# Optimization experiments

Hardware: AMD Instinct MI355X
Metric: run time of the kernel (lower is better)

The kernel has to match this reference:

```python
import jax, jax.numpy as jnp
import numpy as np

N_LAYERS = 2
DIN = 128
DOUT = 128


def _uniform(key, shape, std):
    return jax.random.uniform(key, shape, jnp.float32, -std, std)


def setup_inputs() -> dict:
    key = jax.random.key(0)
    ks = jax.random.split(key, 12)
    B, T, N, F = 2, 8, 10000, DIN
    E = 320000
    x = jax.random.normal(ks[0], (B, T, N, F), jnp.float32)
    edge_index = jax.random.randint(ks[1], (2, E), 0, N, jnp.int64)
    edge_weight = jax.random.uniform(ks[2], (E,), jnp.float32)
    std_w = 1.0 / np.sqrt(DOUT)
    std_p = 1.0 / np.sqrt(DIN)
    std_g = 1.0 / np.sqrt(DIN)  # torch GRUCell init: U(-1/sqrt(H), 1/sqrt(H))
    W0 = _uniform(ks[3], (N_LAYERS, DIN, DOUT), std_w)
    p = _uniform(ks[4], (N_LAYERS, DIN, 1), std_p)
    w_ih = _uniform(ks[5], (N_LAYERS, 3 * DIN, DIN), std_g)
    w_hh = _uniform(ks[6], (N_LAYERS, 3 * DIN, DIN), std_g)
    b_ih = _uniform(ks[7], (N_LAYERS, 3 * DIN), std_g)
    b_hh = _uniform(ks[8], (N_LAYERS, 3 * DIN), std_g)
    bias = jnp.zeros((N_LAYERS, DOUT), jnp.float32)
    return {"x": x, "edge_index": edge_index, "edge_weight": edge_weight,
            "W0": W0, "p": p, "w_ih": w_ih, "w_hh": w_hh,
            "b_ih": b_ih, "b_hh": b_hh, "bias": bias}


def _gru_cell(xg, hg, wih, whh, bih, bhh):
    # torch.nn.GRUCell: gate order r, z, n
    gi = xg @ wih.T + bih
    gh = hg @ whh.T + bhh
    ir, iz, inn = jnp.split(gi, 3, axis=-1)
    hr, hz, hn = jnp.split(gh, 3, axis=-1)
    r = jax.nn.sigmoid(ir + hr)
    z = jax.nn.sigmoid(iz + hz)
    n = jnp.tanh(inn + r * hn)
    return (1.0 - z) * n + z * hg


def _topk_pool(xb, pc, k):
    # xb: [b, N, din], pc: [din, 1] -> [b, k, din]
    scores = (xb @ pc)[..., 0] / jnp.linalg.norm(pc)  # [b, N]
    vals, idx = jax.lax.top_k(scores, k)               # [b, k], sorted desc
    g = jnp.take_along_axis(xb, idx[..., None], axis=1)  # [b, k, din]
    return g * jnp.tanh(vals)[..., None]


def reference(x, edge_index, edge_weight, W0, p, w_ih, w_hh, b_ih, b_hh, bias):
    B, T, N, F = x.shape
    dout = W0.shape[-1]
    # --- GCN symmetric normalization with self-loops (done once, static graph) ---
    src, tgt = edge_index[0], edge_index[1]
    loops = jnp.arange(N, dtype=src.dtype)
    row = jnp.concatenate([src, loops])
    col = jnp.concatenate([tgt, loops])
    w = jnp.concatenate([edge_weight, jnp.ones((N,), x.dtype)])
    deg = jnp.zeros((N,), x.dtype).at[col].add(w)
    dinv = jnp.where(deg > 0, deg ** -0.5, 0.0)
    wn = dinv[row] * w * dinv[col]  # [E+N]

    def step(Ws, xt):
        out = xt  # [b, N, din]
        new_Ws = []
        for c in range(N_LAYERS):
            W = Ws[c]  # [b, din, dout]
            din = W.shape[1]
            pooled = _topk_pool(out, p[c], dout)                 # [b, dout, din]
            hg = W.transpose(0, 2, 1).reshape(B * dout, din)     # (b dout) din
            xg = pooled.reshape(B * dout, din)
            hg = _gru_cell(xg, hg, w_ih[c], w_hh[c], b_ih[c], b_hh[c])
            W = hg.reshape(B, dout, din).transpose(0, 2, 1)      # [b, din, dout]
            o = jnp.einsum('bnd,bde->bne', out, W)               # [b, N, dout]
            # gather-scale-scatter propagation (aggr='add')
            m = o[:, row, :] * wn[None, :, None]                 # [b, E+N, dout]
            o = jnp.zeros((B, N, dout), x.dtype).at[:, col, :].add(m)
            o = o + bias[c]
            out = jax.nn.relu(o)
            new_Ws.append(W)
        return tuple(new_Ws), out

    Ws0 = tuple(jnp.broadcast_to(W0[c], (B,) + W0[c].shape) for c in range(N_LAYERS))
    _, outs = jax.lax.scan(step, Ws0, jnp.moveaxis(x, 1, 0))
    return outs[-1]  # output at final step, [b, N, hidden]
```

## Files before the change

### kernel.cpp

```cpp
#include <hip/hip_runtime.h>
#include <hip/hip_bf16.h>
#include <math.h>


#define BB 2
#define TT 8
#define FF 128
#define GG 384
#define BINS 8192
#define CAP 512

typedef float v4f __attribute__((ext_vector_type(4)));

__device__ __forceinline__ float bf2f(unsigned short u) {
  return __uint_as_float((unsigned)u << 16);
}
__device__ __forceinline__ unsigned short f2bf(float f) {
  unsigned x = __float_as_uint(f);
  unsigned r = ((x >> 16) & 1u) + 0x7fffu;
  return (unsigned short)((x + r) >> 16);
}

__global__ void prep_kernel(const int* __restrict__ ei32, int E, int* __restrict__ flag,
                            const float* __restrict__ p, float* __restrict__ pinv) {
  if (blockIdx.x == 0) {
    int step = E / 256;
    int e = threadIdx.x * step;
    if (ei32[2 * e + 1] != 0) *flag = 1;
  } else {
    int c = blockIdx.x - 1, tid = threadIdx.x;
    float s = 0.f;
    if (tid < 128) { float v = p[c * FF + tid]; s = v * v; }
    for (int o = 32; o; o >>= 1) s += __shfl_xor(s, o, 64);
    __shared__ float red[4];
    if ((tid & 63) == 0) red[tid >> 6] = s;
    __syncthreads();
    if (tid == 0) pinv[c] = 1.0f / sqrtf(red[0] + red[1] + red[2] + red[3]);
  }
}

__device__ __forceinline__ void edge_fetch(const void* ei, int is32, int E,
                                           int e, const float* ew,
                                           int& row, int& col, float& w) {
  if (e < E) {
    if (is32) {
      const int* p = (const int*)ei;
      row = p[e]; col = p[E + e];
    } else {
      const long long* p = (const long long*)ei;
      row = (int)p[e]; col = (int)p[(long long)E + e];
    }
    w = ew[e];
  } else {
    row = col = e - E; w = 1.0f;
  }
}

__global__ void hist_kernel(const void* ei, const int* flag, int E, int N,
                            const float* __restrict__ ew,
                            float* __restrict__ deg, int* __restrict__ counts) {
  int e = blockIdx.x * 256 + threadIdx.x;
  if (e >= E + N) return;
  int row, col; float w;
  edge_fetch(ei, *flag, E, e, ew, row, col, w);
  atomicAdd(&deg[col], w);
  atomicAdd(&counts[col], 1);
}

__global__ __launch_bounds__(1024) void scan_kernel(
    const int* __restrict__ counts, const float* __restrict__ deg,
    int* __restrict__ offsets, float* __restrict__ dinv, int N, int EN) {
  __shared__ int wtot[16];
  int tid = threadIdx.x, lane = tid & 63, wid = tid >> 6;
  int base = tid * 10;
  int lc[10]; int s10 = 0;
#pragma unroll
  for (int q = 0; q < 10; ++q) {
    int idx = base + q;
    int cv = (idx < N) ? counts[idx] : 0;
    lc[q] = cv; s10 += cv;
    if (idx < N) {
      float d = deg[idx];
      dinv[idx] = (d > 0.f) ? 1.0f / sqrtf(d) : 0.f;
    }
  }
  int s = s10;
#pragma unroll
  for (int off = 1; off <= 32; off <<= 1) {
    int v = __shfl_up(s, off, 64);
    if (lane >= off) s += v;
  }
  if (lane == 63) wtot[wid] = s;
  __syncthreads();
  int pre = 0;
  for (int w2 = 0; w2 < wid; ++w2) pre += wtot[w2];
  int run = pre + s - s10;
#pragma unroll
  for (int q = 0; q < 10; ++q) {
    int idx = base + q;
    if (idx < N) { offsets[idx] = run; run += lc[q]; }
  }
  if (tid == 0) offsets[N] = EN;
}

__global__ void scatter_kernel(const void* ei, const int* flag, int E, int N,
                               const float* __restrict__ ew,
                               const float* __restrict__ dinv,
                               const int* __restrict__ offs,
                               int* __restrict__ cursors,
                               int2* __restrict__ ep) {
  int e = blockIdx.x * 256 + threadIdx.x;
  if (e >= E + N) return;
  int row, col; float w;
  edge_fetch(ei, *flag, E, e, ew, row, col, w);
  int pos = atomicAdd(&cursors[col], 1);
  ep[offs[col] + pos] = make_int2(row, __float_as_int(dinv[row] * w * dinv[col]));
}

template <int SRC_BF16>
__global__ __launch_bounds__(256) void prop_kernel(
    const void* __restrict__ srcv, size_t s_tstride, size_t s_bstride,
    float* __restrict__ dst, size_t d_tstride, size_t d_bstride,
    const int2* __restrict__ ep, const int* __restrict__ offs,
    const float* __restrict__ p, const float* __restrict__ pinv,
    unsigned long long* __restrict__ keys, int* __restrict__ hist,
    int N, int NG, int t8) {
  constexpr int PER = SRC_BF16 ? 8 : 4;
  constexpr int RSU = SRC_BF16 ? 16 : 32;
  int lid = blockIdx.x;
  int t, s;
  if (t8) { t = lid & 7; s = lid >> 3; } else { t = 0; s = lid; }
  int fq = s / NG, vg = s - fq * NG;
  int lane = threadIdx.x & 63;
  int e = lane >> 3, sub = lane & 7;
  int v = vg * 4 + (threadIdx.x >> 6);
  if (v >= N) return;
  int e0 = offs[v], e1 = offs[v + 1];
  size_t o0 = (size_t)t * s_tstride, o1 = o0 + s_bstride;
  const uint4* g0;
  const uint4* g1;
  if constexpr (SRC_BF16) {
    g0 = (const uint4*)((const unsigned short*)srcv + o0);
    g1 = (const uint4*)((const unsigned short*)srcv + o1);
  } else {
    g0 = (const uint4*)((const float*)srcv + o0);
    g1 = (const uint4*)((const float*)srcv + o1);
  }
  int fqs = fq * 8;
  float acc0[PER], acc1[PER];
#pragma unroll
  for (int q = 0; q < PER; ++q) { acc0[q] = 0.f; acc1[q] = 0.f; }
  for (int base = e0; base < e1; base += 64) {
    int cnt = e1 - base; if (cnt > 64) cnt = 64;
    int2 m = make_int2(0, 0);
    if (lane < cnt) m = ep[base + lane];
    for (int i = 0; i < cnt; i += 8) {
      int srcl = i + e;
      int row = __shfl(m.x, srcl, 64);
      float wv = __int_as_float(__shfl(m.y, srcl, 64));
      if (srcl >= cnt) wv = 0.f;
      size_t r = (size_t)row * RSU + fqs + sub;
      uint4 ra = g0[r], rb = g1[r];
      if constexpr (SRC_BF16) {
        acc0[0] += wv * bf2f(ra.x & 0xffff); acc0[1] += wv * bf2f(ra.x >> 16);
        acc0[2] += wv * bf2f(ra.y & 0xffff); acc0[3] += wv * bf2f(ra.y >> 16);
        acc0[4] += wv * bf2f(ra.z & 0xffff); acc0[5] += wv * bf2f(ra.z >> 16);
        acc0[6] += wv * bf2f(ra.w & 0xffff); acc0[7] += wv * bf2f(ra.w >> 16);
        acc1[0] += wv * bf2f(rb.x & 0xffff); acc1[1] += wv * bf2f(rb.x >> 16);
        acc1[2] += wv * bf2f(rb.y & 0xffff); acc1[3] += wv * bf2f(rb.y >> 16);
        acc1[4] += wv * bf2f(rb.z & 0xffff); acc1[5] += wv * bf2f(rb.z >> 16);
        acc1[6] += wv * bf2f(rb.w & 0xffff); acc1[7] += wv * bf2f(rb.w >> 16);
      } else {
        acc0[0] += wv * __uint_as_float(ra.x);
        acc0[1] += wv * __uint_as_float(ra.y);
        acc0[2] += wv * __uint_as_float(ra.z);
        acc0[3] += wv * __uint_as_float(ra.w);
        acc1[0] += wv * __uint_as_float(rb.x);
        acc1[1] += wv * __uint_as_float(rb.y);
        acc1[2] += wv * __uint_as_float(rb.z);
        acc1[3] += wv * __uint_as_float(rb.w);
      }
    }
  }
#pragma unroll
  for (int mk = 8; mk <= 32; mk <<= 1) {
#pragma unroll
    for (int q = 0; q < PER; ++q) {
      acc0[q] += __shfl_xor(acc0[q], mk, 64);
      acc1[q] += __shfl_xor(acc1[q], mk, 64);
    }
  }
  if (e < 2) {
    float* ob = dst + (size_t)t * d_tstride + (e ? d_bstride : 0);
    float* av = e ? acc1 : acc0;
    size_t fo = (size_t)v * FF + fq * (PER * 8) + sub * PER;
    v4f st0 = {av[0], av[1], av[2], av[3]};
    __builtin_nontemporal_store(st0, (v4f*)(ob + fo));
    if constexpr (SRC_BF16) {
      v4f st1 = {av[4], av[5], av[6], av[7]};
      __builtin_nontemporal_store(st1, (v4f*)(ob + fo + 4));
    }
  }
  if constexpr (!SRC_BF16) {
    if (p && fq == 0) {
      int half = lane >> 5, i32 = lane & 31;
      const v4f* xrow = (const v4f*)(half ? g1 : g0);
      v4f xv = __builtin_nontemporal_load(xrow + (size_t)v * 32 + i32);
      float4 pp = ((const float4*)p)[i32];
      float sc = xv.x * pp.x + xv.y * pp.y + xv.z * pp.z + xv.w * pp.w;
#pragma unroll
      for (int o = 1; o <= 16; o <<= 1) sc += __shfl_xor(sc, o, 64);
      if (i32 == 0) {
        float ss = sc * (*pinv);
        unsigned u = __float_as_uint(ss);
        u = (u & 0x80000000u) ? ~u : (u | 0x80000000u);
        int tb = t * 2 + half;
        keys[(size_t)tb * N + v] = ((unsigned long long)u << 32) | (unsigned)(~v);
        atomicAdd(&hist[tb * BINS + (u >> 19)], 1);
      }
    }
  }
}

__device__ __forceinline__ unsigned long long shfl_xor_u64(unsigned long long x,
                                                           int m) {
  unsigned lo = (unsigned)x, hi = (unsigned)(x >> 32);
  lo = __shfl_xor(lo, m, 64);
  hi = __shfl_xor(hi, m, 64);
  return ((unsigned long long)hi << 32) | lo;
}

__global__ __launch_bounds__(1024) void selectsort_kernel(
    const unsigned long long* __restrict__ keys, const int* __restrict__ hist,
    int N, int* __restrict__ idx_sel, float* __restrict__ gate_sel) {
  int tb = blockIdx.y * 2 + blockIdx.x, tid = threadIdx.x;
  int lane = tid & 63, wid = tid >> 6;
  const int* h = hist + tb * BINS;
  __shared__ int wtot[16];
  __shared__ unsigned long long cand[CAP];
  __shared__ int sT, ncnt;
  int base = tid * 8;
  int lc[8]; int local = 0;
#pragma unroll
  for (int q = 0; q < 8; ++q) { lc[q] = h[base + q]; local += lc[q]; }
  if (tid == 0) ncnt = 0;
  int s = local;
#pragma unroll
  for (int off = 1; off <= 32; off <<= 1) {
    int v = __shfl_down(s, off, 64);
    if (lane + off < 64) s += v;
  }
  if (lane == 0) wtot[wid] = s;
  __syncthreads();
  int above_w = 0;
  for (int w2 = wid + 1; w2 < 16; ++w2) above_w += wtot[w2];
  int incl = above_w + s;
  int above = incl - local;
  if (above < 128 && incl >= 128) {
    int cnt = above;
#pragma unroll
    for (int q = 7; q >= 0; --q) {
      int c = lc[q];
      if (cnt + c >= 128) { sT = base + q; break; }
      cnt += c;
    }
  }
  __syncthreads();
  int T = sT;
  for (int i = tid; i < N; i += 1024) {
    unsigned long long kk = keys[(size_t)tb * N + i];
    if ((int)(kk >> 51) >= T) {
      int pos = atomicAdd(&ncnt, 1);
      if (pos < CAP) cand[pos] = kk;
    }
  }
  __syncthreads();
  if (tid < 64) {
    int nc = ncnt < CAP ? ncnt : CAP;
    unsigned long long v[8];
#pragma unroll
    for (int r = 0; r < 8; ++r) {
      int e = r * 64 + lane;
      v[r] = (e < nc) ? cand[e] : 0ULL;
    }
    for (int k = 2; k <= 512; k <<= 1)
      for (int j = k >> 1; j > 0; j >>= 1) {
        if (j >= 64) {
          int rj = j >> 6;
#pragma unroll
          for (int r = 0; r < 8; ++r)
            if (!(r & rj)) {
              int r2 = r | rj;
              bool up = (((r * 64) & k) != 0);
              unsigned long long a = v[r], c = v[r2];
              bool sw = up ? (a > c) : (a < c);
              if (sw) { v[r] = c; v[r2] = a; }
            }
        } else {
#pragma unroll
          for (int r = 0; r < 8; ++r) {
            unsigned long long o = shfl_xor_u64(v[r], j);
            int e = r * 64 + lane;
            bool up = (e & k) != 0;
            bool lower = (lane & j) == 0;
            unsigned long long mn = v[r] < o ? v[r] : o;
            unsigned long long mx = v[r] < o ? o : v[r];
            v[r] = (lower == up) ? mn : mx;
          }
        }
      }
#pragma unroll
    for (int r = 0; r < 2; ++r) {
      int e = r * 64 + lane;
      unsigned long long kk = v[r];
      unsigned n = ~((unsigned)kk);
      unsigned u = (unsigned)(kk >> 32);
      float sc = (u & 0x80000000u) ? __uint_as_float(u & 0x7FFFFFFFu)
                                   : __uint_as_float(~u);
      idx_sel[tb * 128 + e] = (int)n;
      gate_sel[tb * 128 + e] = tanhf(sc);
    }
  }
}

template <int SRC_BF16>
__global__ __launch_bounds__(256) void wchain_kernel(
    const void* __restrict__ srcv, size_t src_tstride, size_t src_bstride,
    const int* __restrict__ idx_sel, const float* __restrict__ gate_sel,
    const float* __restrict__ Winit,
    const float* __restrict__ wih, const float* __restrict__ whh,
    const float* __restrict__ bih, const float* __restrict__ bhh,
    float* __restrict__ snap) {
  int b = blockIdx.x, j0 = blockIdx.y * 2;
  int tid = threadIdx.x, side = tid >> 7, kl = tid & 127;
  __shared__ float pooled[2][FF];
  __shared__ float hbuf[2][FF];
  __shared__ float ghbuf[3][2][FF];
  for (int e = tid; e < 2 * FF; e += 256) {
    int j = e >> 7, m = e & 127;
    hbuf[j][m] = Winit[m * FF + j0 + j];
  }
  float b0 = side ? bhh[kl] : bih[kl];
  float b1 = side ? bhh[FF + kl] : bih[FF + kl];
  float b2 = side ? bhh[2 * FF + kl] : bih[2 * FF + kl];
  const float* wmat = side ? whh : wih;
  const float4* w0p = (const float4*)(wmat + (size_t)(0 * FF + kl) * FF);
  const float4* w1p = (const float4*)(wmat + (size_t)(1 * FF + kl) * FF);
  const float4* w2p = (const float4*)(wmat + (size_t)(2 * FF + kl) * FF);
  for (int t = 0; t < TT; ++t) {
    int tb = t * 2 + b;
    __syncthreads();
    for (int e = tid; e < 2 * FF; e += 256) {
      int j = e >> 7, m = e & 127;
      int n = idx_sel[tb * 128 + j0 + j];
      float g = gate_sel[tb * 128 + j0 + j];
      size_t off = (size_t)t * src_tstride + (size_t)b * src_bstride +
                   (size_t)n * FF + m;
      float xv;
      if constexpr (SRC_BF16) xv = bf2f(((const unsigned short*)srcv)[off]);
      else                    xv = ((const float*)srcv)[off];
      pooled[j][m] = xv * g;
    }
    __syncthreads();
    const float4* vsrc = (const float4*)(side ? &hbuf[0][0] : &pooled[0][0]);
    float acc0[2] = {}, acc1[2] = {}, acc2[2] = {};
    for (int mq = 0; mq < 32; ++mq) {
      float4 w0 = w0p[mq], w1 = w1p[mq], w2 = w2p[mq];
#pragma unroll
      for (int j = 0; j < 2; ++j) {
        float4 v = vsrc[j * 32 + mq];
        acc0[j] += v.x * w0.x + v.y * w0.y + v.z * w0.z + v.w * w0.w;
        acc1[j] += v.x * w1.x + v.y * w1.y + v.z * w1.z + v.w * w1.w;
        acc2[j] += v.x * w2.x + v.y * w2.y + v.z * w2.z + v.w * w2.w;
      }
    }
    if (side) {
#pragma unroll
      for (int j = 0; j < 2; ++j) {
        ghbuf[0][j][kl] = acc0[j] + b0;
        ghbuf[1][j][kl] = acc1[j] + b1;
        ghbuf[2][j][kl] = acc2[j] + b2;
      }
    }
    __syncthreads();
    if (!side) {
#pragma unroll
      for (int j = 0; j < 2; ++j) {
        float rr = 1.0f / (1.0f + expf(-(acc0[j] + b0 + ghbuf[0][j][kl])));
        float zz = 1.0f / (1.0f + expf(-(acc1[j] + b1 + ghbuf[1][j][kl])));
        float nn = tanhf(acc2[j] + b2 + rr * ghbuf[2][j][kl]);
        float h = hbuf[j][kl];
        float hn = (1.0f - zz) * nn + zz * h;
        hbuf[j][kl] = hn;
        snap[((size_t)tb * FF + kl) * FF + j0 + j] = hn;
      }
    }
  }
}

__global__ __launch_bounds__(256) void gemm_kernel(
    const float* __restrict__ A, size_t a_tstride, size_t a_bstride,
    const float* __restrict__ Wsnap, const float* __restrict__ bias,
    float* __restrict__ outf, unsigned short* __restrict__ outb,
    size_t o_tstride, size_t o_bstride,
    const float* __restrict__ p1, const float* __restrict__ pinv1,
    unsigned long long* __restrict__ keys, int* __restrict__ hist, int N) {
  int nb = blockIdx.x, b = blockIdx.y, t = blockIdx.z;
  int tb = t * 2 + b;
  __shared__ float As[128][33];
  __shared__ float Bs[32][128];
  __shared__ float spart[128][17];
  __shared__ float p1s[128];
  int tid = threadIdx.x;
  int tc = tid & 15, tr = tid >> 4;
  if (p1 && tid < 128) p1s[tid] = p1[tid];
  float acc[8][8] = {};
  const float* Ab = A + (size_t)t * a_tstride + (size_t)b * a_bstride;
  const float* Wb = Wsnap + (size_t)tb * FF * FF;
  for (int kc = 0; kc < 4; ++kc) {
    int k0 = kc * 32;
    __syncthreads();
    for (int e = tid; e < 128 * 32; e += 256) {
      int r = e >> 5, kk = e & 31;
      int n = nb * 128 + r;
      As[r][kk] = (n < N) ? Ab[(size_t)n * FF + k0 + kk] : 0.f;
    }
    for (int e = tid; e < 32 * 128; e += 256) {
      int r = e >> 7, dd = e & 127;
      Bs[r][dd] = Wb[(k0 + r) * FF + dd];
    }
    __syncthreads();
#pragma unroll 4
    for (int kk = 0; kk < 32; ++kk) {
      float av[8];
#pragma unroll
      for (int i = 0; i < 8; ++i) av[i] = As[tr * 8 + i][kk];
      const float4* brow = (const float4*)Bs[kk];
      float4 b0 = brow[tc * 2], b1 = brow[tc * 2 + 1];
      float bv[8] = {b0.x, b0.y, b0.z, b0.w, b1.x, b1.y, b1.z, b1.w};
#pragma unroll
      for (int i = 0; i < 8; ++i)
#pragma unroll
        for (int j = 0; j < 8; ++j) acc[i][j] += av[i] * bv[j];
    }
  }
  float bb[8];
#pragma unroll
  for (int j = 0; j < 8; ++j) bb[j] = bias[tc * 8 + j];
  size_t obase = (size_t)t * o_tstride + (size_t)b * o_bstride;
#pragma unroll
  for (int i = 0; i < 8; ++i) {
    int n = nb * 128 + tr * 8 + i;
    float v[8]; float part = 0.f;
#pragma unroll
    for (int j = 0; j < 8; ++j) {
      v[j] = fmaxf(acc[i][j] + bb[j], 0.f);
      if (p1) part += v[j] * p1s[tc * 8 + j];
    }
    if (n < N) {
      if (outb) {
        unsigned short* dst = outb + obase + (size_t)n * FF + tc * 8;
        uint4 pk;
        pk.x = (unsigned)f2bf(v[0]) | ((unsigned)f2bf(v[1]) << 16);
        pk.y = (unsigned)f2bf(v[2]) | ((unsigned)f2bf(v[3]) << 16);
        pk.z = (unsigned)f2bf(v[4]) | ((unsigned)f2bf(v[5]) << 16);
        pk.w = (unsigned)f2bf(v[6]) | ((unsigned)f2bf(v[7]) << 16);
        *(uint4*)dst = pk;
      } else {
        float4* dst = (float4*)(outf + obase + (size_t)n * FF + tc * 8);
        dst[0] = make_float4(v[0], v[1], v[2], v[3]);
        dst[1] = make_float4(v[4], v[5], v[6], v[7]);
      }
    }
    if (p1) spart[tr * 8 + i][tc] = part;
  }
  if (p1) {
    __syncthreads();
    if (tid < 128) {
      int n = nb * 128 + tid;
      if (n < N) {
        float s = 0.f;
#pragma unroll
        for (int q = 0; q < 16; ++q) s += spart[tid][q];
        s *= *pinv1;
        unsigned u = __float_as_uint(s);
        u = (u & 0x80000000u) ? ~u : (u | 0x80000000u);
        keys[(size_t)tb * N + n] = ((unsigned long long)u << 32) | (unsigned)(~n);
        atomicAdd(&hist[tb * BINS + (u >> 19)], 1);
      }
    }
  }
}

extern "C" void kernel_launch(void* const* d_in, const int* in_sizes, int n_in,
                              void* d_out, int out_size, void* d_ws, size_t ws_size,
                              hipStream_t stream) {
  const float* x   = (const float*)d_in[0];
  const void*  ei  = d_in[1];
  const float* ew  = (const float*)d_in[2];
  const float* W0  = (const float*)d_in[3];
  const float* p   = (const float*)d_in[4];
  const float* wih = (const float*)d_in[5];
  const float* whh = (const float*)d_in[6];
  const float* bih = (const float*)d_in[7];
  const float* bhh = (const float*)d_in[8];
  const float* bias= (const float*)d_in[9];

  const int E  = in_sizes[2];
  const int N  = in_sizes[0] / (BB * TT * FF);
  const int EN = E + N;
  const size_t NF = (size_t)N * FF;
  const int NG = (N + 3) / 4;

  char* w = (char*)d_ws;
  auto alloc = [&](size_t bytes) -> char* {
    char* r = w; w += (bytes + 255) & ~(size_t)255; return r;
  };
  char* zbeg = w;
  float* deg      = (float*)alloc((size_t)N * 4);
  int*   counts   = (int*)  alloc((size_t)N * 4);
  int*   cursors  = (int*)  alloc((size_t)N * 4);
  int*   flag     = (int*)  alloc(4);
  int*   hist     = (int*)  alloc((size_t)2 * TT * BB * BINS * 4);
  char* zend = w;
  int*   offsets  = (int*)  alloc((size_t)(N + 1) * 4);
  float* dinv     = (float*)alloc((size_t)N * 4);
  float* pinv     = (float*)alloc(2 * 4);
  int2*  ep       = (int2*) alloc((size_t)EN * 8);
  unsigned long long* keys0 = (unsigned long long*)alloc((size_t)TT * BB * N * 8);
  unsigned long long* keys1 = (unsigned long long*)alloc((size_t)TT * BB * N * 8);
  int*   idx0     = (int*)  alloc((size_t)TT * BB * 128 * 4);
  float* gate0    = (float*)alloc((size_t)TT * BB * 128 * 4);
  int*   idx1     = (int*)  alloc((size_t)TT * BB * 128 * 4);
  float* gate1    = (float*)alloc((size_t)TT * BB * 128 * 4);
  float* W0snap   = (float*)alloc((size_t)TT * BB * FF * FF * 4);
  float* W1snap   = (float*)alloc((size_t)TT * BB * FF * FF * 4);
  float* xp       = (float*)alloc((size_t)TT * BB * NF * 4);
  unsigned short* act0 = (unsigned short*)alloc((size_t)TT * BB * NF * 2);
  float* xq       = (float*)alloc((size_t)BB * NF * 4);
  int* hist0 = hist;
  int* hist1 = hist + (size_t)TT * BB * BINS;

  hipMemsetAsync(zbeg, 0, (size_t)(zend - zbeg), stream);

  prep_kernel<<<3, 256, 0, stream>>>((const int*)ei, E, flag, p, pinv);
  hist_kernel<<<(EN + 255) / 256, 256, 0, stream>>>(ei, flag, E, N, ew, deg, counts);
  scan_kernel<<<1, 1024, 0, stream>>>(counts, deg, offsets, dinv, N, EN);
  scatter_kernel<<<(EN + 255) / 256, 256, 0, stream>>>(ei, flag, E, N, ew, dinv,
                                                       offsets, cursors, ep);

  prop_kernel<0><<<NG * 4 * TT, 256, 0, stream>>>(
      x, NF, (size_t)TT * NF, xp, (size_t)BB * NF, NF,
      ep, offsets, p, pinv, keys0, hist0, N, NG, 1);

  selectsort_kernel<<<dim3(BB, TT), 1024, 0, stream>>>(
      keys0, hist0, N, idx0, gate0);

  wchain_kernel<0><<<dim3(BB, 64), 256, 0, stream>>>(
      x, NF, (size_t)TT * NF, idx0, gate0, W0,
      wih, whh, bih, bhh, W0snap);

  gemm_kernel<<<dim3((N + 127) / 128, BB, TT), 256, 0, stream>>>(
      xp, (size_t)BB * NF, NF, W0snap, bias,
      nullptr, act0, (size_t)BB * NF, NF,
      p + FF, pinv + 1, keys1, hist1, N);

  selectsort_kernel<<<dim3(BB, TT), 1024, 0, stream>>>(
      keys1, hist1, N, idx1, gate1);

  wchain_kernel<1><<<dim3(BB, 64), 256, 0, stream>>>(
      act0, (size_t)BB * NF, NF, idx1, gate1, W0 + FF * FF,
      wih + (size_t)GG * FF, whh + (size_t)GG * FF,
      bih + GG, bhh + GG, W1snap);

  prop_kernel<1><<<NG * 2, 256, 0, stream>>>(
      act0 + (size_t)(TT - 1) * BB * NF, 0, NF, xq, 0, NF,
      ep, offsets, nullptr, nullptr, nullptr, nullptr, N, NG, 0);

  gemm_kernel<<<dim3((N + 127) / 128, BB, 1), 256, 0, stream>>>(
      xq, 0, NF, W1snap + (size_t)(TT - 1) * BB * FF * FF, bias + FF,
      (float*)d_out, nullptr, 0, NF,
      nullptr, nullptr, nullptr, nullptr, N);
}
```

Measured before the change: 823.3 us.

## Split GRU weight chain into batched input-gate GEMM and lightweight recurrent kernel

The input-side GRU projection (pooled @ w_ih^T + b_ih) does not depend on the recurrent state, so it is hoisted out of the sequential time loop into a separate tiled GEMM kernel covering all timesteps and batches at once. The remaining recurrent kernel only computes the hidden-side projection and the gate math, using one column per block and 384 threads across all three gates. This gives more parallelism and less work on the serial chain. The cost is an extra launch and a global buffer round-trip for the precomputed input gates.

```diff
diff --git a/kernel.cpp b/kernel.cpp
--- a/kernel.cpp
+++ b/kernel.cpp
@@ -324,77 +324,105 @@
 }
 
 template <int SRC_BF16>
-__global__ __launch_bounds__(256) void wchain_kernel(
+__global__ __launch_bounds__(256) void gipre_kernel(
     const void* __restrict__ srcv, size_t src_tstride, size_t src_bstride,
     const int* __restrict__ idx_sel, const float* __restrict__ gate_sel,
+    const float* __restrict__ wih, const float* __restrict__ bih,
+    float* __restrict__ gi) {
+  int g = blockIdx.x, b = blockIdx.y, t = blockIdx.z;
+  int tb = t * 2 + b, gbase = g * 128;
+  __shared__ float As[128][33];
+  __shared__ float Bs[128][33];
+  __shared__ int s_idx[128];
+  __shared__ float s_gate[128];
+  int tid = threadIdx.x;
+  int tc = tid & 15, tr = tid >> 4;
+  if (tid < 128) {
+    s_idx[tid] = idx_sel[tb * 128 + tid];
+    s_gate[tid] = gate_sel[tb * 128 + tid];
+  }
+  float acc[8][8] = {};
+  const char* srcb = (const char*)srcv;
+  size_t sbase = (size_t)t * src_tstride + (size_t)b * src_bstride;
+  for (int kc = 0; kc < 4; ++kc) {
+    int k0 = kc * 32;
+    __syncthreads();
+    for (int e = tid; e < 128 * 32; e += 256) {
+      int j = e >> 5, kk = e & 31;
+      size_t off = sbase + (size_t)s_idx[j] * FF + k0 + kk;
+      float xv;
+      if constexpr (SRC_BF16) xv = bf2f(((const unsigned short*)srcb)[off]);
+      else                    xv = ((const float*)srcb)[off];
+      As[j][kk] = xv * s_gate[j];
+    }
+    for (int e = tid; e < 128 * 32; e += 256) {
+      int r = e >> 5, kk = e & 31;
+      Bs[r][kk] = wih[(size_t)(gbase + r) * FF + k0 + kk];
+    }
+    __syncthreads();
+#pragma unroll 4
+    for (int kk = 0; kk < 32; ++kk) {
+      float av[8], bv[8];
+#pragma unroll
+      for (int i = 0; i < 8; ++i) av[i] = As[tr * 8 + i][kk];
+#pragma unroll
+      for (int j = 0; j < 8; ++j) bv[j] = Bs[tc * 8 + j][kk];
+#pragma unroll
+      for (int i = 0; i < 8; ++i)
+#pragma unroll
+        for (int j = 0; j < 8; ++j) acc[i][j] += av[i] * bv[j];
+    }
+  }
+  float bb[8];
+#pragma unroll
+  for (int j = 0; j < 8; ++j) bb[j] = bih[gbase + tc * 8 + j];
+#pragma unroll
+  for (int i = 0; i < 8; ++i) {
+    float* dst = gi + (size_t)(tb * 128 + tr * 8 + i) * GG + gbase + tc * 8;
+    float4* d4 = (float4*)dst;
+    d4[0] = make_float4(acc[i][0] + bb[0], acc[i][1] + bb[1],
+                        acc[i][2] + bb[2], acc[i][3] + bb[3]);
+    d4[1] = make_float4(acc[i][4] + bb[4], acc[i][5] + bb[5],
+                        acc[i][6] + bb[6], acc[i][7] + bb[7]);
+  }
+}
+
+__global__ __launch_bounds__(384) void wlite_kernel(
+    const float* __restrict__ gi,
     const float* __restrict__ Winit,
-    const float* __restrict__ wih, const float* __restrict__ whh,
-    const float* __restrict__ bih, const float* __restrict__ bhh,
+    const float* __restrict__ whh, const float* __restrict__ bhh,
     float* __restrict__ snap) {
-  int b = blockIdx.x, j0 = blockIdx.y * 2;
-  int tid = threadIdx.x, side = tid >> 7, kl = tid & 127;
-  __shared__ float pooled[2][FF];
-  __shared__ float hbuf[2][FF];
-  __shared__ float ghbuf[3][2][FF];
-  for (int e = tid; e < 2 * FF; e += 256) {
-    int j = e >> 7, m = e & 127;
-    hbuf[j][m] = Winit[m * FF + j0 + j];
-  }
-  float b0 = side ? bhh[kl] : bih[kl];
-  float b1 = side ? bhh[FF + kl] : bih[FF + kl];
-  float b2 = side ? bhh[2 * FF + kl] : bih[2 * FF + kl];
-  const float* wmat = side ? whh : wih;
-  const float4* w0p = (const float4*)(wmat + (size_t)(0 * FF + kl) * FF);
-  const float4* w1p = (const float4*)(wmat + (size_t)(1 * FF + kl) * FF);
-  const float4* w2p = (const float4*)(wmat + (size_t)(2 * FF + kl) * FF);
+  int b = blockIdx.x, j = blockIdx.y;
+  int tid = threadIdx.x, g = tid >> 7, k = tid & 127;
+  __shared__ float hbuf[FF];
+  __shared__ float gh3[3][FF];
+  if (tid < 128) hbuf[tid] = Winit[tid * FF + j];
+  float bh = bhh[g * 128 + k];
+  const float4* wrow = (const float4*)(whh + (size_t)(g * 128 + k) * FF);
+  __syncthreads();
   for (int t = 0; t < TT; ++t) {
     int tb = t * 2 + b;
-    __syncthreads();
-    for (int e = tid; e < 2 * FF; e += 256) {
-      int j = e >> 7, m = e & 127;
-      int n = idx_sel[tb * 128 + j0 + j];
-      float g = gate_sel[tb * 128 + j0 + j];
-      size_t off = (size_t)t * src_tstride + (size_t)b * src_bstride +
-                   (size_t)n * FF + m;
-      float xv;
-      if constexpr (SRC_BF16) xv = bf2f(((const unsigned short*)srcv)[off]);
-      else                    xv = ((const float*)srcv)[off];
-      pooled[j][m] = xv * g;
-    }
-    __syncthreads();
-    const float4* vsrc = (const float4*)(side ? &hbuf[0][0] : &pooled[0][0]);
-    float acc0[2] = {}, acc1[2] = {}, acc2[2] = {};
+    const float4* h4 = (const float4*)hbuf;
+    float acc = 0.f;
+#pragma unroll 8
     for (int mq = 0; mq < 32; ++mq) {
-      float4 w0 = w0p[mq], w1 = w1p[mq], w2 = w2p[mq];
-#pragma unroll
-      for (int j = 0; j < 2; ++j) {
-        float4 v = vsrc[j * 32 + mq];
-        acc0[j] += v.x * w0.x + v.y * w0.y + v.z * w0.z + v.w * w0.w;
-        acc1[j] += v.x * w1.x + v.y * w1.y + v.z * w1.z + v.w * w1.w;
-        acc2[j] += v.x * w2.x + v.y * w2.y + v.z * w2.z + v.w * w2.w;
-      }
-    }
-    if (side) {
-#pragma unroll
-      for (int j = 0; j < 2; ++j) {
-        ghbuf[0][j][kl] = acc0[j] + b0;
-        ghbuf[1][j][kl] = acc1[j] + b1;
-        ghbuf[2][j][kl] = acc2[j] + b2;
-      }
-    }
-    __syncthreads();
-    if (!side) {
-#pragma unroll
-      for (int j = 0; j < 2; ++j) {
-        float rr = 1.0f / (1.0f + expf(-(acc0[j] + b0 + ghbuf[0][j][kl])));
-        float zz = 1.0f / (1.0f + expf(-(acc1[j] + b1 + ghbuf[1][j][kl])));
-        float nn = tanhf(acc2[j] + b2 + rr * ghbuf[2][j][kl]);
-        float h = hbuf[j][kl];
-        float hn = (1.0f - zz) * nn + zz * h;
-        hbuf[j][kl] = hn;
-        snap[((size_t)tb * FF + kl) * FF + j0 + j] = hn;
-      }
-    }
+      float4 hv = h4[mq], wv = wrow[mq];
+      acc += hv.x * wv.x + hv.y * wv.y + hv.z * wv.z + hv.w * wv.w;
+    }
+    gh3[g][k] = acc + bh;
+    __syncthreads();
+    if (g == 0) {
+      size_t row = (size_t)(tb * 128 + j) * GG;
+      float gir = gi[row + k], giz = gi[row + 128 + k], gin = gi[row + 256 + k];
+      float rr = 1.0f / (1.0f + expf(-(gir + gh3[0][k])));
+      float zz = 1.0f / (1.0f + expf(-(giz + gh3[1][k])));
+      float nn = tanhf(gin + rr * gh3[2][k]);
+      float h = hbuf[k];
+      float hn = (1.0f - zz) * nn + zz * h;
+      hbuf[k] = hn;
+      snap[((size_t)tb * FF + k) * FF + j] = hn;
+    }
+    __syncthreads();
   }
 }
 
@@ -535,6 +563,7 @@
   float* gate1    = (float*)alloc((size_t)TT * BB * 128 * 4);
   float* W0snap   = (float*)alloc((size_t)TT * BB * FF * FF * 4);
   float* W1snap   = (float*)alloc((size_t)TT * BB * FF * FF * 4);
+  float* gibuf    = (float*)alloc((size_t)TT * BB * 128 * GG * 4);
   float* xp       = (float*)alloc((size_t)TT * BB * NF * 4);
   unsigned short* act0 = (unsigned short*)alloc((size_t)TT * BB * NF * 2);
   float* xq       = (float*)alloc((size_t)BB * NF * 4);
@@ -556,9 +585,10 @@
   selectsort_kernel<<<dim3(BB, TT), 1024, 0, stream>>>(
       keys0, hist0, N, idx0, gate0);
 
-  wchain_kernel<0><<<dim3(BB, 64), 256, 0, stream>>>(
-      x, NF, (size_t)TT * NF, idx0, gate0, W0,
-      wih, whh, bih, bhh, W0snap);
+  gipre_kernel<0><<<dim3(3, BB, TT), 256, 0, stream>>>(
+      x, NF, (size_t)TT * NF, idx0, gate0, wih, bih, gibuf);
+  wlite_kernel<<<dim3(BB, 128), 384, 0, stream>>>(
+      gibuf, W0, whh, bhh, W0snap);
 
   gemm_kernel<<<dim3((N + 127) / 128, BB, TT), 256, 0, stream>>>(
       xp, (size_t)BB * NF, NF, W0snap, bias,
@@ -568,10 +598,11 @@
   selectsort_kernel<<<dim3(BB, TT), 1024, 0, stream>>>(
       keys1, hist1, N, idx1, gate1);
 
-  wchain_kernel<1><<<dim3(BB, 64), 256, 0, stream>>>(
-      act0, (size_t)BB * NF, NF, idx1, gate1, W0 + FF * FF,
-      wih + (size_t)GG * FF, whh + (size_t)GG * FF,
-      bih + GG, bhh + GG, W1snap);
+  gipre_kernel<1><<<dim3(3, BB, TT), 256, 0, stream>>>(
+      act0, (size_t)BB * NF, NF, idx1, gate1,
+      wih + (size_t)GG * FF, bih + GG, gibuf);
+  wlite_kernel<<<dim3(BB, 128), 384, 0, stream>>>(
+      gibuf, W0 + FF * FF, whh + (size_t)GG * FF, bhh + GG, W1snap);
 
   prop_kernel<1><<<NG * 2, 256, 0, stream>>>(
       act0 + (size_t)(TT - 1) * BB * NF, 0, NF, xq, 0, NF,
```

New measurement: 806.6 us. -2.0%, faster.
